# Kernel optimization log

Measured on AMD Instinct MI355X. Metric: run time of the kernel, lower is better.

Reference implementation:

```python
import jax, jax.numpy as jnp
import numpy as np

MSE_WEIGHT = 0.7
CORR_WEIGHT = 0.3
EPS = 1e-8
B, L = 256, 65536


def setup_inputs() -> dict:
    key = jax.random.key(0)
    k1, k2 = jax.random.split(key)
    y_pred = jax.random.normal(k1, (B, L), dtype=jnp.float32)
    y_true = jax.random.normal(k2, (B, L), dtype=jnp.float32)
    return {"y_pred": y_pred, "y_true": y_true}


def reference(y_pred, y_true):
    # MSE over all elements (nn.MSELoss default 'mean')
    mse_loss = jnp.mean((y_pred - y_true) ** 2)

    # Vectorized per-sample Pearson correlation (original loops over batch)
    xm = y_true - jnp.mean(y_true, axis=1, keepdims=True)   # [B, L]
    ym = y_pred - jnp.mean(y_pred, axis=1, keepdims=True)   # [B, L]
    r_num = jnp.sum(xm * ym, axis=1)                        # [B]
    r_den = jnp.sqrt(jnp.sum(xm * xm, axis=1) * jnp.sum(ym * ym, axis=1))
    r_den = jnp.maximum(r_den, EPS)
    r = r_num / r_den                                       # [B]
    corr_loss = jnp.mean(1.0 - r)

    total_loss = MSE_WEIGHT * mse_loss + CORR_WEIGHT * corr_loss
    return total_loss.reshape(1)  # original returns shape-[1] tensor
```

## Files before the change

### kernel.cpp

```cpp
#include <hip/hip_runtime.h>

#define B_ROWS   256
#define L_COLS   65536
#define SLICES   8
#define THREADS  256
#define NBLOCKS  (B_ROWS * SLICES)
#define V_ROW    (L_COLS / 4)
#define V_SLICE  (V_ROW / SLICES)

__global__ __launch_bounds__(THREADS)
void signal_loss_partials(const float4* __restrict__ pred,
                          const float4* __restrict__ trgt,
                          float* __restrict__ ws)
{
    const int bid   = blockIdx.x;
    const int row   = bid >> 3;
    const int slice = bid & (SLICES - 1);
    const size_t base = (size_t)row * V_ROW + (size_t)slice * V_SLICE + threadIdx.x;
    const float4* P = pred + base;
    const float4* T = trgt + base;

    float sp = 0.f, st = 0.f, spp = 0.f, stt = 0.f, spt = 0.f, sd2 = 0.f;

    float4 a0, a1, c0, c1;
    float4 b0, b1, d0, d1;

#define LOAD_A(bk) do { \
    a0 = P[((bk)*2+0)*THREADS]; a1 = P[((bk)*2+1)*THREADS]; \
    c0 = T[((bk)*2+0)*THREADS]; c1 = T[((bk)*2+1)*THREADS]; } while (0)
#define LOAD_B(bk) do { \
    b0 = P[((bk)*2+0)*THREADS]; b1 = P[((bk)*2+1)*THREADS]; \
    d0 = T[((bk)*2+0)*THREADS]; d1 = T[((bk)*2+1)*THREADS]; } while (0)

#define ACC1(p, t) do { \
    sp  += (p).x + (p).y + (p).z + (p).w; \
    st  += (t).x + (t).y + (t).z + (t).w; \
    spp += (p).x*(p).x + (p).y*(p).y + (p).z*(p).z + (p).w*(p).w; \
    stt += (t).x*(t).x + (t).y*(t).y + (t).z*(t).z + (t).w*(t).w; \
    spt += (p).x*(t).x + (p).y*(t).y + (p).z*(t).z + (p).w*(t).w; \
    { const float dx=(p).x-(t).x, dy=(p).y-(t).y, dz=(p).z-(t).z, dw=(p).w-(t).w; \
      sd2 += dx*dx + dy*dy + dz*dz + dw*dw; } } while (0)

    LOAD_A(0);
    LOAD_B(1);
    ACC1(a0, c0); ACC1(a1, c1);
    LOAD_A(2);
    ACC1(b0, d0); ACC1(b1, d1);
    LOAD_B(3);
    ACC1(a0, c0); ACC1(a1, c1);
    ACC1(b0, d0); ACC1(b1, d1);

#undef LOAD_A
#undef LOAD_B
#undef ACC1

    #pragma unroll
    for (int off = 32; off >= 1; off >>= 1) {
        sp  += __shfl_down(sp,  off);
        st  += __shfl_down(st,  off);
        spp += __shfl_down(spp, off);
        stt += __shfl_down(stt, off);
        spt += __shfl_down(spt, off);
        sd2 += __shfl_down(sd2, off);
    }

    __shared__ float red[4][6];
    const int lane = threadIdx.x & 63;
    const int wave = threadIdx.x >> 6;
    if (lane == 0) {
        red[wave][0] = sp;  red[wave][1] = st;  red[wave][2] = spp;
        red[wave][3] = stt; red[wave][4] = spt; red[wave][5] = sd2;
    }
    __syncthreads();
    if (threadIdx.x == 0) {
        float* dst = ws + (size_t)bid * 8;
        #pragma unroll
        for (int k = 0; k < 6; ++k)
            dst[k] = red[0][k] + red[1][k] + red[2][k] + red[3][k];
        dst[6] = 0.f; dst[7] = 0.f;
    }
}

__global__ __launch_bounds__(B_ROWS)
void signal_loss_finalize(const float4* __restrict__ ws4,
                          float* __restrict__ out)
{
    const int row = threadIdx.x;

    float4 lo[SLICES], hi[SLICES];
    #pragma unroll
    for (int sl = 0; sl < SLICES; ++sl) {
        const size_t rec = ((size_t)row * SLICES + sl) * 2;
        lo[sl] = ws4[rec + 0];
        hi[sl] = ws4[rec + 1];
    }

    double s0=0.0, s1=0.0, s2=0.0, s3=0.0, s4=0.0, s5=0.0;
    #pragma unroll
    for (int sl = 0; sl < SLICES; ++sl) {
        s0 += (double)lo[sl].x;
        s1 += (double)lo[sl].y;
        s2 += (double)lo[sl].z;
        s3 += (double)lo[sl].w;
        s4 += (double)hi[sl].x;
        s5 += (double)hi[sl].y;
    }

    const double n = (double)L_COLS;
    const double num   = s4 - s0 * s1 / n;
    const double den_t = s3 - s1 * s1 / n;
    const double den_p = s2 - s0 * s0 / n;
    double den = sqrt(den_t * den_p);
    den = den > 1e-8 ? den : 1e-8;
    double romr = 1.0 - num / den;
    double sd   = s5;

    #pragma unroll
    for (int off = 32; off >= 1; off >>= 1) {
        romr += __shfl_down(romr, off);
        sd   += __shfl_down(sd,   off);
    }
    __shared__ double w0[4], w1[4];
    const int lane = threadIdx.x & 63;
    const int wave = threadIdx.x >> 6;
    if (lane == 0) { w0[wave] = romr; w1[wave] = sd; }
    __syncthreads();
    if (threadIdx.x == 0) {
        const double corr = (w0[0] + w0[1] + w0[2] + w0[3]) / (double)B_ROWS;
        const double mse  = (w1[0] + w1[1] + w1[2] + w1[3])
                          / ((double)B_ROWS * (double)L_COLS);
        out[0] = (float)(0.7 * mse + 0.3 * corr);
    }
}

extern "C" void kernel_launch(void* const* d_in, const int* in_sizes, int n_in,
                              void* d_out, int out_size, void* d_ws, size_t ws_size,
                              hipStream_t stream) {
    const float4* pred = (const float4*)d_in[0];
    const float4* trgt = (const float4*)d_in[1];
    float* ws  = (float*)d_ws;
    float* out = (float*)d_out;

    signal_loss_partials<<<NBLOCKS, THREADS, 0, stream>>>(pred, trgt, ws);
    signal_loss_finalize<<<1, B_ROWS, 0, stream>>>((const float4*)ws, out);
}
```

Before: 28.88 us.

## Derive squared error from existing moments and deepen load pipelining

Drops the separate sum of squared differences and rebuilds it in the finalize step as spp + stt - 2*spt, which removes four subtracts and four FMAs per element pair plus one shuffle reduction chain. The load schedule now keeps three float4 batches in flight instead of two, and launch bounds request 8 blocks per CU. Recovering the squared error from moments in float partials can lose precision through cancellation. The kernel is memory-bound, so the compute savings may matter little.

```diff
diff --git a/kernel.cpp b/kernel.cpp
--- a/kernel.cpp
+++ b/kernel.cpp
@@ -8,7 +8,7 @@
 #define V_ROW    (L_COLS / 4)
 #define V_SLICE  (V_ROW / SLICES)
 
-__global__ __launch_bounds__(THREADS)
+__global__ __launch_bounds__(THREADS, 8)
 void signal_loss_partials(const float4* __restrict__ pred,
                           const float4* __restrict__ trgt,
                           float* __restrict__ ws)
@@ -20,38 +20,33 @@
     const float4* P = pred + base;
     const float4* T = trgt + base;
 
-    float sp = 0.f, st = 0.f, spp = 0.f, stt = 0.f, spt = 0.f, sd2 = 0.f;
+    float sp = 0.f, st = 0.f, spp = 0.f, stt = 0.f, spt = 0.f;
 
-    float4 a0, a1, c0, c1;
-    float4 b0, b1, d0, d1;
+    float4 a0, a1, at0, at1;
+    float4 b0, b1, bt0, bt1;
+    float4 g0, g1, gt0, gt1;
 
-#define LOAD_A(bk) do { \
-    a0 = P[((bk)*2+0)*THREADS]; a1 = P[((bk)*2+1)*THREADS]; \
-    c0 = T[((bk)*2+0)*THREADS]; c1 = T[((bk)*2+1)*THREADS]; } while (0)
-#define LOAD_B(bk) do { \
-    b0 = P[((bk)*2+0)*THREADS]; b1 = P[((bk)*2+1)*THREADS]; \
-    d0 = T[((bk)*2+0)*THREADS]; d1 = T[((bk)*2+1)*THREADS]; } while (0)
+#define LOADB(r0, r1, rt0, rt1, bk) do { \
+    r0  = P[((bk)*2+0)*THREADS]; r1  = P[((bk)*2+1)*THREADS]; \
+    rt0 = T[((bk)*2+0)*THREADS]; rt1 = T[((bk)*2+1)*THREADS]; } while (0)
 
 #define ACC1(p, t) do { \
     sp  += (p).x + (p).y + (p).z + (p).w; \
     st  += (t).x + (t).y + (t).z + (t).w; \
     spp += (p).x*(p).x + (p).y*(p).y + (p).z*(p).z + (p).w*(p).w; \
     stt += (t).x*(t).x + (t).y*(t).y + (t).z*(t).z + (t).w*(t).w; \
-    spt += (p).x*(t).x + (p).y*(t).y + (p).z*(t).z + (p).w*(t).w; \
-    { const float dx=(p).x-(t).x, dy=(p).y-(t).y, dz=(p).z-(t).z, dw=(p).w-(t).w; \
-      sd2 += dx*dx + dy*dy + dz*dz + dw*dw; } } while (0)
+    spt += (p).x*(t).x + (p).y*(t).y + (p).z*(t).z + (p).w*(t).w; } while (0)
 
-    LOAD_A(0);
-    LOAD_B(1);
-    ACC1(a0, c0); ACC1(a1, c1);
-    LOAD_A(2);
-    ACC1(b0, d0); ACC1(b1, d1);
-    LOAD_B(3);
-    ACC1(a0, c0); ACC1(a1, c1);
-    ACC1(b0, d0); ACC1(b1, d1);
+    LOADB(a0, a1, at0, at1, 0);
+    LOADB(b0, b1, bt0, bt1, 1);
+    LOADB(g0, g1, gt0, gt1, 2);
+    ACC1(a0, at0); ACC1(a1, at1);
+    LOADB(a0, a1, at0, at1, 3);
+    ACC1(b0, bt0); ACC1(b1, bt1);
+    ACC1(g0, gt0); ACC1(g1, gt1);
+    ACC1(a0, at0); ACC1(a1, at1);
 
-#undef LOAD_A
-#undef LOAD_B
+#undef LOADB
 #undef ACC1
 
     #pragma unroll
@@ -61,23 +56,22 @@
         spp += __shfl_down(spp, off);
         stt += __shfl_down(stt, off);
         spt += __shfl_down(spt, off);
-        sd2 += __shfl_down(sd2, off);
     }
 
-    __shared__ float red[4][6];
+    __shared__ float red[4][5];
     const int lane = threadIdx.x & 63;
     const int wave = threadIdx.x >> 6;
     if (lane == 0) {
         red[wave][0] = sp;  red[wave][1] = st;  red[wave][2] = spp;
-        red[wave][3] = stt; red[wave][4] = spt; red[wave][5] = sd2;
+        red[wave][3] = stt; red[wave][4] = spt;
     }
     __syncthreads();
     if (threadIdx.x == 0) {
         float* dst = ws + (size_t)bid * 8;
         #pragma unroll
-        for (int k = 0; k < 6; ++k)
+        for (int k = 0; k < 5; ++k)
             dst[k] = red[0][k] + red[1][k] + red[2][k] + red[3][k];
-        dst[6] = 0.f; dst[7] = 0.f;
+        dst[5] = 0.f; dst[6] = 0.f; dst[7] = 0.f;
     }
 }
 
@@ -95,7 +89,7 @@
         hi[sl] = ws4[rec + 1];
     }
 
-    double s0=0.0, s1=0.0, s2=0.0, s3=0.0, s4=0.0, s5=0.0;
+    double s0=0.0, s1=0.0, s2=0.0, s3=0.0, s4=0.0;
     #pragma unroll
     for (int sl = 0; sl < SLICES; ++sl) {
         s0 += (double)lo[sl].x;
@@ -103,7 +97,6 @@
         s2 += (double)lo[sl].z;
         s3 += (double)lo[sl].w;
         s4 += (double)hi[sl].x;
-        s5 += (double)hi[sl].y;
     }
 
     const double n = (double)L_COLS;
@@ -113,7 +106,7 @@
     double den = sqrt(den_t * den_p);
     den = den > 1e-8 ? den : 1e-8;
     double romr = 1.0 - num / den;
-    double sd   = s5;
+    double sd   = s2 + s3 - 2.0 * s4;
 
     #pragma unroll
     for (int off = 32; off >= 1; off >>= 1) {
```

Measured after the change: 29.21 us. Within noise of the previous version (+1.1%).
